# Performance work log

Measured on AMD Instinct MI355X. Metric: run time of the kernel, lower is better.

The kernel has to match this reference:

```python
import jax, jax.numpy as jnp
import numpy as np

B, N, D, H = 8, 384, 256, 1024

def setup_inputs() -> dict:
    key = jax.random.key(0)
    ks = jax.random.split(key, 8)
    x = jax.random.normal(ks[0], (B, N, D), jnp.float32)
    adj = jnp.ones((B, N, N), jnp.float32)
    box_num = jax.random.randint(ks[1], (B, 1), 1, N + 1).astype(jnp.int64)
    box_num = box_num.at[0, 0].set(N)  # original code assumes max(box_num) == N
    fc1_w = jax.random.normal(ks[2], (H, D), jnp.float32) * (1.0 / np.sqrt(D))
    fc1_b = jnp.zeros((H,), jnp.float32)
    fc2_w = jax.random.normal(ks[3], (D, H), jnp.float32) * (1.0 / np.sqrt(H))
    fc2_b = jnp.zeros((D,), jnp.float32)
    learn_w = jax.random.uniform(ks[4], (D,), jnp.float32)  # uniform_(0,1) init
    return {"x": x, "adj": adj, "box_num": box_num,
            "fc1_w": fc1_w, "fc1_b": fc1_b, "fc2_w": fc2_w, "fc2_b": fc2_b,
            "learn_w": learn_w}

def reference(x, adj, box_num, fc1_w, fc1_b, fc2_w, fc2_b, learn_w):
    # mlp: fc2(relu(fc1(x)))  -> x_hat (B,N,D)
    x_hat = jnp.maximum(x @ fc1_w.T + fc1_b, 0.0) @ fc2_w.T + fc2_b
    # dynamic mask: -1 where either node i or j is padding, 0 otherwise
    valid = jnp.arange(N)[None, :] < box_num            # (B,N)
    pair_valid = valid[:, None, :] & valid[:, :, None]  # (B,N,N)
    mask = jnp.where(pair_valid, 0.0, -1.0)             # (B,N,N)
    # pairwise weighted L1 distance: einsum('bijd,d->bij', |x_i - x_j| + mask, w)
    # mask broadcasts over d, so its contribution is mask * sum(w) (same math,
    # avoids a second (B,N,N,D) materialization)
    absdiff = jnp.abs(x_hat[:, :, None, :] - x_hat[:, None, :, :])  # (B,N,N,D)
    dist = jnp.einsum('bijd,d->bij', absdiff, learn_w) + mask * jnp.sum(learn_w)
    out = jax.nn.leaky_relu(dist, negative_slope=0.01)
    out = out - jnp.max(out, axis=-1, keepdims=True)
    soft_adj = adj * jnp.exp(out)
    soft_adj = soft_adj / jnp.sum(soft_adj, axis=-1, keepdims=True) + 1e-10
    return soft_adj, x_hat
```

## Files before the change

kernel.cpp:

```cpp
#include <hip/hip_runtime.h>
#include <math.h>

#define B_ 8
#define N_ 384
#define D_ 256
#define H_ 1024

typedef __bf16 bh;
typedef __bf16 bf16x8 __attribute__((ext_vector_type(8)));
typedef float  f32x4  __attribute__((ext_vector_type(4)));
typedef _Float16 h2 __attribute__((ext_vector_type(2)));

#define LDK 40

#if __has_builtin(__builtin_amdgcn_fdot2)
#define FDOT2(a,b,c) __builtin_amdgcn_fdot2((a),(b),(c),false)
#else
#define FDOT2(a,b,c) ((c) + (float)(a).x*(float)(b).x + (float)(a).y*(float)(b).y)
#endif

__device__ inline h2 habs2(h2 x) {
    unsigned u = __builtin_bit_cast(unsigned, x) & 0x7fff7fffu;
    return __builtin_bit_cast(h2, u);
}

__device__ inline void split2(float v, bh& h, bh& l) {
    h = (bh)v;
    l = (bh)(v - (float)h);
}

__device__ inline int load_boxnum(const int* __restrict__ p, int b) {
    bool is64 = ((p[1] | p[3] | p[5] | p[7]) == 0);
    return is64 ? p[2 * b] : p[b];
}

__global__ __launch_bounds__(256) void gemm1_kernel(
        const float* __restrict__ A,
        const float* __restrict__ W,
        const float* __restrict__ bias,
        bh* __restrict__ Ch, bh* __restrict__ Cl)
{
    __shared__ __align__(16) bh AhS[64 * LDK], AlS[64 * LDK], WhS[64 * LDK], WlS[64 * LDK];
    const int tid = threadIdx.x;
    const int m0 = blockIdx.y * 64, n0 = blockIdx.x * 64;
    const int r = tid >> 2, kq = (tid & 3) * 8;
    const int lane = tid & 63, wv_ = tid >> 6;
    const int wm = (wv_ & 1) * 32, wn = (wv_ >> 1) * 32;
    const int l15 = lane & 15, q = lane >> 4;

    f32x4 acc[2][2] = {};
    for (int k0 = 0; k0 < 256; k0 += 32) {
        const float* ap = A + (size_t)(m0 + r) * 256 + k0 + kq;
        const float* wp = W + (size_t)(n0 + r) * 256 + k0 + kq;
        float4 a0 = *(const float4*)ap;
        float4 a1 = *(const float4*)(ap + 4);
        float4 w0 = *(const float4*)wp;
        float4 w1 = *(const float4*)(wp + 4);
        float av[8] = {a0.x, a0.y, a0.z, a0.w, a1.x, a1.y, a1.z, a1.w};
        float wf[8] = {w0.x, w0.y, w0.z, w0.w, w1.x, w1.y, w1.z, w1.w};
        bf16x8 ah, al, wh, wl;
        #pragma unroll
        for (int i = 0; i < 8; i++) {
            bh h, l;
            split2(av[i], h, l); ah[i] = h; al[i] = l;
            split2(wf[i], h, l); wh[i] = h; wl[i] = l;
        }
        __syncthreads();
        *(bf16x8*)&AhS[r * LDK + kq] = ah;  *(bf16x8*)&AlS[r * LDK + kq] = al;
        *(bf16x8*)&WhS[r * LDK + kq] = wh;  *(bf16x8*)&WlS[r * LDK + kq] = wl;
        __syncthreads();
        bf16x8 fah[2], fal[2], fwh[2], fwl[2];
        #pragma unroll
        for (int mi = 0; mi < 2; mi++) {
            int row = wm + mi * 16 + l15;
            fah[mi] = *(const bf16x8*)&AhS[row * LDK + q * 8];
            fal[mi] = *(const bf16x8*)&AlS[row * LDK + q * 8];
        }
        #pragma unroll
        for (int ni = 0; ni < 2; ni++) {
            int row = wn + ni * 16 + l15;
            fwh[ni] = *(const bf16x8*)&WhS[row * LDK + q * 8];
            fwl[ni] = *(const bf16x8*)&WlS[row * LDK + q * 8];
        }
        #pragma unroll
        for (int mi = 0; mi < 2; mi++)
            #pragma unroll
            for (int ni = 0; ni < 2; ni++) {
                acc[mi][ni] = __builtin_amdgcn_mfma_f32_16x16x32_bf16(fah[mi], fwh[ni], acc[mi][ni], 0, 0, 0);
                acc[mi][ni] = __builtin_amdgcn_mfma_f32_16x16x32_bf16(fah[mi], fwl[ni], acc[mi][ni], 0, 0, 0);
                acc[mi][ni] = __builtin_amdgcn_mfma_f32_16x16x32_bf16(fal[mi], fwh[ni], acc[mi][ni], 0, 0, 0);
            }
    }
    #pragma unroll
    for (int ni = 0; ni < 2; ni++) {
        int col = n0 + wn + ni * 16 + l15;
        float bb = bias[col];
        #pragma unroll
        for (int mi = 0; mi < 2; mi++)
            #pragma unroll
            for (int reg = 0; reg < 4; reg++) {
                int row = m0 + wm + mi * 16 + q * 4 + reg;
                float v = fmaxf(acc[mi][ni][reg] + bb, 0.f);
                bh h, l; split2(v, h, l);
                size_t off = (size_t)row * H_ + col;
                Ch[off] = h; Cl[off] = l;
            }
    }
}

__global__ __launch_bounds__(128) void gemm2_kernel(
        const bh* __restrict__ Ah_, const bh* __restrict__ Al_,
        const float* __restrict__ W,
        const float* __restrict__ bias,
        float* __restrict__ C)
{
    __shared__ __align__(16) bh AhS[64 * LDK], AlS[64 * LDK], WhS[32 * LDK], WlS[32 * LDK];
    const int tid = threadIdx.x;
    const int m0 = blockIdx.y * 64, n0 = blockIdx.x * 32;
    const int lane = tid & 63, wv_ = tid >> 6;
    const int wm = wv_ * 32;
    const int l15 = lane & 15, q = lane >> 4;
    const int ra = tid >> 1, ka = (tid & 1) * 16;
    const int rw = tid >> 2, kw = (tid & 3) * 8;

    f32x4 acc[2][2] = {};
    for (int k0 = 0; k0 < 1024; k0 += 32) {
        const bh* ahp = Ah_ + (size_t)(m0 + ra) * H_ + k0 + ka;
        const bh* alp = Al_ + (size_t)(m0 + ra) * H_ + k0 + ka;
        bf16x8 h0 = *(const bf16x8*)ahp, h1 = *(const bf16x8*)(ahp + 8);
        bf16x8 l0 = *(const bf16x8*)alp, l1 = *(const bf16x8*)(alp + 8);
        const float* wp = W + (size_t)(n0 + rw) * H_ + k0 + kw;
        float4 w0 = *(const float4*)wp, w1 = *(const float4*)(wp + 4);
        float wf[8] = {w0.x, w0.y, w0.z, w0.w, w1.x, w1.y, w1.z, w1.w};
        bf16x8 wh, wl;
        #pragma unroll
        for (int i = 0; i < 8; i++) { bh h, l; split2(wf[i], h, l); wh[i] = h; wl[i] = l; }
        __syncthreads();
        *(bf16x8*)&AhS[ra * LDK + ka] = h0;  *(bf16x8*)&AhS[ra * LDK + ka + 8] = h1;
        *(bf16x8*)&AlS[ra * LDK + ka] = l0;  *(bf16x8*)&AlS[ra * LDK + ka + 8] = l1;
        *(bf16x8*)&WhS[rw * LDK + kw] = wh;  *(bf16x8*)&WlS[rw * LDK + kw] = wl;
        __syncthreads();
        bf16x8 fah[2], fal[2], fwh[2], fwl[2];
        #pragma unroll
        for (int mi = 0; mi < 2; mi++) {
            int row = wm + mi * 16 + l15;
            fah[mi] = *(const bf16x8*)&AhS[row * LDK + q * 8];
            fal[mi] = *(const bf16x8*)&AlS[row * LDK + q * 8];
        }
        #pragma unroll
        for (int ni = 0; ni < 2; ni++) {
            int row = ni * 16 + l15;
            fwh[ni] = *(const bf16x8*)&WhS[row * LDK + q * 8];
            fwl[ni] = *(const bf16x8*)&WlS[row * LDK + q * 8];
        }
        #pragma unroll
        for (int mi = 0; mi < 2; mi++)
            #pragma unroll
            for (int ni = 0; ni < 2; ni++) {
                acc[mi][ni] = __builtin_amdgcn_mfma_f32_16x16x32_bf16(fah[mi], fwh[ni], acc[mi][ni], 0, 0, 0);
                acc[mi][ni] = __builtin_amdgcn_mfma_f32_16x16x32_bf16(fah[mi], fwl[ni], acc[mi][ni], 0, 0, 0);
                acc[mi][ni] = __builtin_amdgcn_mfma_f32_16x16x32_bf16(fal[mi], fwh[ni], acc[mi][ni], 0, 0, 0);
            }
    }
    #pragma unroll
    for (int ni = 0; ni < 2; ni++) {
        int col = n0 + ni * 16 + l15;
        float bb = bias[col];
        #pragma unroll
        for (int mi = 0; mi < 2; mi++)
            #pragma unroll
            for (int reg = 0; reg < 4; reg++) {
                int row = m0 + wm + mi * 16 + q * 4 + reg;
                C[(size_t)row * D_ + col] = acc[mi][ni][reg] + bb;
            }
    }
}

#define DLP 68
__global__ __launch_bounds__(256) void dist_kernel(const float* __restrict__ xhat,
                                                   const float* __restrict__ w,
                                                   const int* __restrict__ box_num,
                                                   float* __restrict__ dist) {
    __shared__ __align__(16) unsigned XiU[16 * DLP];
    __shared__ __align__(16) unsigned XjU[16 * DLP];
    const int bidx = blockIdx.x;
    const int b = bidx / 21;
    int p = bidx % 21;
    int ti = 0;
    while (p >= 6 - ti) { p -= 6 - ti; ti++; }
    const int tj = ti + p;
    const int i0 = ti * 64, j0 = tj * 64;

    const int tid = threadIdx.x;
    const int tx = tid & 15, ty = tid >> 4;
    const int lane = tid & 63;
    const int r = tid >> 2, kq = (tid & 3) * 8;
    const int kq2 = (tid & 3) * 4;

    float sumw = w[lane] + w[lane + 64] + w[lane + 128] + w[lane + 192];
    #pragma unroll
    for (int off = 32; off > 0; off >>= 1) sumw += __shfl_xor(sumw, off);

    const float* xb = xhat + (size_t)b * N_ * D_;
    float acc[4][4] = {};

    for (int k0 = 0; k0 < D_; k0 += 32) {
        h2 wk2[16];
        #pragma unroll
        for (int c = 0; c < 16; c++) {
            float2 wp = *(const float2*)&w[k0 + 2 * c];
            wk2[c] = (h2){(_Float16)wp.x, (_Float16)wp.y};
        }
        const float* ip = xb + (size_t)(i0 + r) * D_ + k0 + kq;
        const float* jp = xb + (size_t)(j0 + r) * D_ + k0 + kq;
        float4 i0v = *(const float4*)ip, i1v = *(const float4*)(ip + 4);
        float4 j0v = *(const float4*)jp, j1v = *(const float4*)(jp + 4);
        float fi[8] = {i0v.x, i0v.y, i0v.z, i0v.w, i1v.x, i1v.y, i1v.z, i1v.w};
        float fj[8] = {j0v.x, j0v.y, j0v.z, j0v.w, j1v.x, j1v.y, j1v.z, j1v.w};
        __syncthreads();
        #pragma unroll
        for (int c = 0; c < 4; c++) {
            h2 hi = (h2){(_Float16)fi[2 * c], (_Float16)fi[2 * c + 1]};
            h2 hj = (h2){(_Float16)fj[2 * c], (_Float16)fj[2 * c + 1]};
            XiU[(kq2 + c) * DLP + r] = __builtin_bit_cast(unsigned, hi);
            XjU[(kq2 + c) * DLP + r] = __builtin_bit_cast(unsigned, hj);
        }
        __syncthreads();
        #pragma unroll
        for (int k2 = 0; k2 < 16; k2++) {
            uint4 ar = *(const uint4*)&XiU[k2 * DLP + ty * 4];
            uint4 br = *(const uint4*)&XjU[k2 * DLP + tx * 4];
            h2 ai[4] = {__builtin_bit_cast(h2, ar.x), __builtin_bit_cast(h2, ar.y),
                        __builtin_bit_cast(h2, ar.z), __builtin_bit_cast(h2, ar.w)};
            h2 bj[4] = {__builtin_bit_cast(h2, br.x), __builtin_bit_cast(h2, br.y),
                        __builtin_bit_cast(h2, br.z), __builtin_bit_cast(h2, br.w)};
            h2 wv = wk2[k2];
            #pragma unroll
            for (int ii = 0; ii < 4; ii++)
                #pragma unroll
                for (int jj = 0; jj < 4; jj++) {
                    h2 d = habs2(ai[ii] - bj[jj]);
                    acc[ii][jj] = FDOT2(d, wv, acc[ii][jj]);
                }
        }
    }

    const int bn = load_boxnum(box_num, b);
    float m[4][4];
    #pragma unroll
    for (int ii = 0; ii < 4; ii++) {
        int i = i0 + ty * 4 + ii;
        bool vi = i < bn;
        #pragma unroll
        for (int jj = 0; jj < 4; jj++) {
            int j = j0 + tx * 4 + jj;
            float v = acc[ii][jj];
            if (!(vi && (j < bn))) v -= sumw;
            m[ii][jj] = v > 0.f ? v : 0.01f * v;
        }
    }
    #pragma unroll
    for (int ii = 0; ii < 4; ii++) {
        int i = i0 + ty * 4 + ii;
        float4 o = {m[ii][0], m[ii][1], m[ii][2], m[ii][3]};
        *(float4*)&dist[((size_t)b * N_ + i) * N_ + j0 + tx * 4] = o;
    }
    #pragma unroll
    for (int jj = 0; jj < 4; jj++) {
        int j = j0 + tx * 4 + jj;
        float4 o = {m[0][jj], m[1][jj], m[2][jj], m[3][jj]};
        *(float4*)&dist[((size_t)b * N_ + j) * N_ + i0 + ty * 4] = o;
    }
}

__global__ __launch_bounds__(256) void softmax_kernel(float* __restrict__ sa,
                                                      const float* __restrict__ adj) {
    const int row = blockIdx.x * 4 + (threadIdx.x >> 6);
    const int t = threadIdx.x & 63;
    float* prow = sa + (size_t)row * N_;
    const float* arow = adj + (size_t)row * N_;
    float v[6];
    float m = -1e30f;
    #pragma unroll
    for (int qq = 0; qq < 6; qq++) { v[qq] = prow[t + qq * 64]; m = fmaxf(m, v[qq]); }
    #pragma unroll
    for (int off = 32; off > 0; off >>= 1) m = fmaxf(m, __shfl_xor(m, off));
    float e[6];
    float s = 0.f;
    #pragma unroll
    for (int qq = 0; qq < 6; qq++) { e[qq] = arow[t + qq * 64] * expf(v[qq] - m); s += e[qq]; }
    #pragma unroll
    for (int off = 32; off > 0; off >>= 1) s += __shfl_xor(s, off);
    float inv = 1.0f / s;
    #pragma unroll
    for (int qq = 0; qq < 6; qq++) prow[t + qq * 64] = e[qq] * inv + 1e-10f;
}

extern "C" void kernel_launch(void* const* d_in, const int* in_sizes, int n_in,
                              void* d_out, int out_size, void* d_ws, size_t ws_size,
                              hipStream_t stream) {
    const float* x       = (const float*)d_in[0];
    const float* adj     = (const float*)d_in[1];
    const int*   box_num = (const int*)d_in[2];
    const float* fc1_w   = (const float*)d_in[3];
    const float* fc1_b   = (const float*)d_in[4];
    const float* fc2_w   = (const float*)d_in[5];
    const float* fc2_b   = (const float*)d_in[6];
    const float* learn_w = (const float*)d_in[7];

    float* soft_adj = (float*)d_out;
    float* xhat     = (float*)d_out + (size_t)B_ * N_ * N_;

    const int BN = B_ * N_;
    const size_t bytes_per_row = (size_t)H_ * 2 * 2;
    long long mr = (long long)(ws_size / bytes_per_row) & ~63LL;
    int max_rows = (int)((mr > BN) ? BN : mr);
    if (max_rows < 64) max_rows = 64;
    bh* c1h = (bh*)d_ws;
    bh* c1l = c1h + (size_t)max_rows * H_;

    for (int m0 = 0; m0 < BN; m0 += max_rows) {
        int rows = BN - m0; if (rows > max_rows) rows = max_rows;
        dim3 g1(H_ / 64, rows / 64);
        gemm1_kernel<<<g1, 256, 0, stream>>>(x + (size_t)m0 * D_, fc1_w, fc1_b, c1h, c1l);
        dim3 g2(D_ / 32, rows / 64);
        gemm2_kernel<<<g2, 128, 0, stream>>>(c1h, c1l, fc2_w, fc2_b, xhat + (size_t)m0 * D_);
    }

    dist_kernel<<<B_ * 21, 256, 0, stream>>>(xhat, learn_w, box_num, soft_adj);

    softmax_kernel<<<BN / 4, 256, 0, stream>>>(soft_adj, adj);
}
```

Measured before the change: 140.5 us.

## Pre-split operands to bf16 hi/lo, widen GEMM K-tiles, restructure dist kernel

A new split kernel converts x and both weight matrices into bf16 hi/lo pairs once, so the GEMMs no longer redo the split inside their K loops. Both GEMMs now stage 64-wide K tiles per sync, and gemm2 runs 256 threads with one 16-row M tile per wave. gemm2 also writes an fp16 copy of x_hat, which the distance kernel loads in one pass into a 128-row transposed shared tile and processes with 512 threads. The cost is an extra kernel launch and more workspace, and correctness relies on ws_size being large enough for the fixed buffers.

```diff
diff --git a/kernel.cpp b/kernel.cpp
--- a/kernel.cpp
+++ b/kernel.cpp
@@ -8,10 +8,11 @@
 
 typedef __bf16 bh;
 typedef __bf16 bf16x8 __attribute__((ext_vector_type(8)));
+typedef __bf16 bf16x4 __attribute__((ext_vector_type(4)));
 typedef float  f32x4  __attribute__((ext_vector_type(4)));
 typedef _Float16 h2 __attribute__((ext_vector_type(2)));
 
-#define LDK 40
+#define LDB 72
 
 #if __has_builtin(__builtin_amdgcn_fdot2)
 #define FDOT2(a,b,c) __builtin_amdgcn_fdot2((a),(b),(c),false)
@@ -34,62 +35,83 @@
     return is64 ? p[2 * b] : p[b];
 }
 
+__global__ __launch_bounds__(256) void split3_kernel(
+        const float* __restrict__ s0, bh* __restrict__ h0, bh* __restrict__ l0, int n0,
+        const float* __restrict__ s1, bh* __restrict__ h1, bh* __restrict__ l1, int n1,
+        const float* __restrict__ s2, bh* __restrict__ h2_, bh* __restrict__ l2, int n2)
+{
+    const int total = n0 + n1 + n2;
+    for (int qd = blockIdx.x * blockDim.x + threadIdx.x; qd < total; qd += gridDim.x * blockDim.x) {
+        const float* s; bh* ph; bh* pl; int i;
+        if (qd < n0)           { s = s0; ph = h0;  pl = l0; i = qd; }
+        else if (qd < n0 + n1) { s = s1; ph = h1;  pl = l1; i = qd - n0; }
+        else                   { s = s2; ph = h2_; pl = l2; i = qd - n0 - n1; }
+        float4 v = *(const float4*)(s + 4 * (size_t)i);
+        bf16x4 hv, lv; bh hh, ll;
+        split2(v.x, hh, ll); hv[0] = hh; lv[0] = ll;
+        split2(v.y, hh, ll); hv[1] = hh; lv[1] = ll;
+        split2(v.z, hh, ll); hv[2] = hh; lv[2] = ll;
+        split2(v.w, hh, ll); hv[3] = hh; lv[3] = ll;
+        *(bf16x4*)(ph + 4 * (size_t)i) = hv;
+        *(bf16x4*)(pl + 4 * (size_t)i) = lv;
+    }
+}
+
 __global__ __launch_bounds__(256) void gemm1_kernel(
-        const float* __restrict__ A,
-        const float* __restrict__ W,
+        const bh* __restrict__ Ah_, const bh* __restrict__ Al_,
+        const bh* __restrict__ Wh_, const bh* __restrict__ Wl_,
         const float* __restrict__ bias,
         bh* __restrict__ Ch, bh* __restrict__ Cl)
 {
-    __shared__ __align__(16) bh AhS[64 * LDK], AlS[64 * LDK], WhS[64 * LDK], WlS[64 * LDK];
+    __shared__ __align__(16) bh AhS[64 * LDB], AlS[64 * LDB], WhS[64 * LDB], WlS[64 * LDB];
     const int tid = threadIdx.x;
     const int m0 = blockIdx.y * 64, n0 = blockIdx.x * 64;
-    const int r = tid >> 2, kq = (tid & 3) * 8;
+    const int r = tid >> 2, kq = (tid & 3) * 16;
     const int lane = tid & 63, wv_ = tid >> 6;
     const int wm = (wv_ & 1) * 32, wn = (wv_ >> 1) * 32;
     const int l15 = lane & 15, q = lane >> 4;
 
     f32x4 acc[2][2] = {};
-    for (int k0 = 0; k0 < 256; k0 += 32) {
-        const float* ap = A + (size_t)(m0 + r) * 256 + k0 + kq;
-        const float* wp = W + (size_t)(n0 + r) * 256 + k0 + kq;
-        float4 a0 = *(const float4*)ap;
-        float4 a1 = *(const float4*)(ap + 4);
-        float4 w0 = *(const float4*)wp;
-        float4 w1 = *(const float4*)(wp + 4);
-        float av[8] = {a0.x, a0.y, a0.z, a0.w, a1.x, a1.y, a1.z, a1.w};
-        float wf[8] = {w0.x, w0.y, w0.z, w0.w, w1.x, w1.y, w1.z, w1.w};
-        bf16x8 ah, al, wh, wl;
-        #pragma unroll
-        for (int i = 0; i < 8; i++) {
-            bh h, l;
-            split2(av[i], h, l); ah[i] = h; al[i] = l;
-            split2(wf[i], h, l); wh[i] = h; wl[i] = l;
+    for (int k0 = 0; k0 < D_; k0 += 64) {
+        const bh* pah = Ah_ + (size_t)(m0 + r) * D_ + k0 + kq;
+        const bh* pal = Al_ + (size_t)(m0 + r) * D_ + k0 + kq;
+        const bh* pwh = Wh_ + (size_t)(n0 + r) * D_ + k0 + kq;
+        const bh* pwl = Wl_ + (size_t)(n0 + r) * D_ + k0 + kq;
+        bf16x8 ah0 = *(const bf16x8*)pah, ah1 = *(const bf16x8*)(pah + 8);
+        bf16x8 al0 = *(const bf16x8*)pal, al1 = *(const bf16x8*)(pal + 8);
+        bf16x8 wh0 = *(const bf16x8*)pwh, wh1 = *(const bf16x8*)(pwh + 8);
+        bf16x8 wl0 = *(const bf16x8*)pwl, wl1 = *(const bf16x8*)(pwl + 8);
+        __syncthreads();
+        *(bf16x8*)&AhS[r * LDB + kq] = ah0;  *(bf16x8*)&AhS[r * LDB + kq + 8] = ah1;
+        *(bf16x8*)&AlS[r * LDB + kq] = al0;  *(bf16x8*)&AlS[r * LDB + kq + 8] = al1;
+        *(bf16x8*)&WhS[r * LDB + kq] = wh0;  *(bf16x8*)&WhS[r * LDB + kq + 8] = wh1;
+        *(bf16x8*)&WlS[r * LDB + kq] = wl0;  *(bf16x8*)&WlS[r * LDB + kq + 8] = wl1;
+        __syncthreads();
+        #pragma unroll
+        for (int ks = 0; ks < 2; ks++) {
+            const int kb = ks * 32 + q * 8;
+            bf16x8 fah[2], fal[2], fwh[2], fwl[2];
+            #pragma unroll
+            for (int mi = 0; mi < 2; mi++) {
+                int row = wm + mi * 16 + l15;
+                fah[mi] = *(const bf16x8*)&AhS[row * LDB + kb];
+                fal[mi] = *(const bf16x8*)&AlS[row * LDB + kb];
+            }
+            #pragma unroll
+            for (int ni = 0; ni < 2; ni++) {
+                int row = wn + ni * 16 + l15;
+                fwh[ni] = *(const bf16x8*)&WhS[row * LDB + kb];
+                fwl[ni] = *(const bf16x8*)&WlS[row * LDB + kb];
+            }
+            #pragma unroll
+            for (int mi = 0; mi < 2; mi++)
+                #pragma unroll
+                for (int ni = 0; ni < 2; ni++) {
+                    acc[mi][ni] = __builtin_amdgcn_mfma_f32_16x16x32_bf16(fah[mi], fwh[ni], acc[mi][ni], 0, 0, 0);
+                    acc[mi][ni] = __builtin_amdgcn_mfma_f32_16x16x32_bf16(fah[mi], fwl[ni], acc[mi][ni], 0, 0, 0);
+                    acc[mi][ni] = __builtin_amdgcn_mfma_f32_16x16x32_bf16(fal[mi], fwh[ni], acc[mi][ni], 0, 0, 0);
+                }
         }
-        __syncthreads();
-        *(bf16x8*)&AhS[r * LDK + kq] = ah;  *(bf16x8*)&AlS[r * LDK + kq] = al;
-        *(bf16x8*)&WhS[r * LDK + kq] = wh;  *(bf16x8*)&WlS[r * LDK + kq] = wl;
-        __syncthreads();
-        bf16x8 fah[2], fal[2], fwh[2], fwl[2];
-        #pragma unroll
-        for (int mi = 0; mi < 2; mi++) {
-            int row = wm + mi * 16 + l15;
-            fah[mi] = *(const bf16x8*)&AhS[row * LDK + q * 8];
-            fal[mi] = *(const bf16x8*)&AlS[row * LDK + q * 8];
-        }
-        #pragma unroll
-        for (int ni = 0; ni < 2; ni++) {
-            int row = wn + ni * 16 + l15;
-            fwh[ni] = *(const bf16x8*)&WhS[row * LDK + q * 8];
-            fwl[ni] = *(const bf16x8*)&WlS[row * LDK + q * 8];
-        }
-        #pragma unroll
-        for (int mi = 0; mi < 2; mi++)
-            #pragma unroll
-            for (int ni = 0; ni < 2; ni++) {
-                acc[mi][ni] = __builtin_amdgcn_mfma_f32_16x16x32_bf16(fah[mi], fwh[ni], acc[mi][ni], 0, 0, 0);
-                acc[mi][ni] = __builtin_amdgcn_mfma_f32_16x16x32_bf16(fah[mi], fwl[ni], acc[mi][ni], 0, 0, 0);
-                acc[mi][ni] = __builtin_amdgcn_mfma_f32_16x16x32_bf16(fal[mi], fwh[ni], acc[mi][ni], 0, 0, 0);
-            }
     }
     #pragma unroll
     for (int ni = 0; ni < 2; ni++) {
@@ -108,81 +130,75 @@
     }
 }
 
-__global__ __launch_bounds__(128) void gemm2_kernel(
+__global__ __launch_bounds__(256) void gemm2_kernel(
         const bh* __restrict__ Ah_, const bh* __restrict__ Al_,
-        const float* __restrict__ W,
+        const bh* __restrict__ Wh_, const bh* __restrict__ Wl_,
         const float* __restrict__ bias,
-        float* __restrict__ C)
+        float* __restrict__ C, _Float16* __restrict__ C16)
 {
-    __shared__ __align__(16) bh AhS[64 * LDK], AlS[64 * LDK], WhS[32 * LDK], WlS[32 * LDK];
+    __shared__ __align__(16) bh AhS[64 * LDB], AlS[64 * LDB], WhS[32 * LDB], WlS[32 * LDB];
     const int tid = threadIdx.x;
     const int m0 = blockIdx.y * 64, n0 = blockIdx.x * 32;
     const int lane = tid & 63, wv_ = tid >> 6;
-    const int wm = wv_ * 32;
+    const int wm = wv_ * 16;
     const int l15 = lane & 15, q = lane >> 4;
-    const int ra = tid >> 1, ka = (tid & 1) * 16;
-    const int rw = tid >> 2, kw = (tid & 3) * 8;
-
-    f32x4 acc[2][2] = {};
-    for (int k0 = 0; k0 < 1024; k0 += 32) {
-        const bh* ahp = Ah_ + (size_t)(m0 + ra) * H_ + k0 + ka;
-        const bh* alp = Al_ + (size_t)(m0 + ra) * H_ + k0 + ka;
-        bf16x8 h0 = *(const bf16x8*)ahp, h1 = *(const bf16x8*)(ahp + 8);
-        bf16x8 l0 = *(const bf16x8*)alp, l1 = *(const bf16x8*)(alp + 8);
-        const float* wp = W + (size_t)(n0 + rw) * H_ + k0 + kw;
-        float4 w0 = *(const float4*)wp, w1 = *(const float4*)(wp + 4);
-        float wf[8] = {w0.x, w0.y, w0.z, w0.w, w1.x, w1.y, w1.z, w1.w};
-        bf16x8 wh, wl;
-        #pragma unroll
-        for (int i = 0; i < 8; i++) { bh h, l; split2(wf[i], h, l); wh[i] = h; wl[i] = l; }
+    const int r = tid >> 2, kq = (tid & 3) * 16;
+    const int rw = tid >> 3, kw = (tid & 7) * 8;
+
+    f32x4 acc[2] = {};
+    for (int k0 = 0; k0 < H_; k0 += 64) {
+        const bh* pah = Ah_ + (size_t)(m0 + r) * H_ + k0 + kq;
+        const bh* pal = Al_ + (size_t)(m0 + r) * H_ + k0 + kq;
+        const bh* pwh = Wh_ + (size_t)(n0 + rw) * H_ + k0 + kw;
+        const bh* pwl = Wl_ + (size_t)(n0 + rw) * H_ + k0 + kw;
+        bf16x8 ah0 = *(const bf16x8*)pah, ah1 = *(const bf16x8*)(pah + 8);
+        bf16x8 al0 = *(const bf16x8*)pal, al1 = *(const bf16x8*)(pal + 8);
+        bf16x8 wh0 = *(const bf16x8*)pwh;
+        bf16x8 wl0 = *(const bf16x8*)pwl;
         __syncthreads();
-        *(bf16x8*)&AhS[ra * LDK + ka] = h0;  *(bf16x8*)&AhS[ra * LDK + ka + 8] = h1;
-        *(bf16x8*)&AlS[ra * LDK + ka] = l0;  *(bf16x8*)&AlS[ra * LDK + ka + 8] = l1;
-        *(bf16x8*)&WhS[rw * LDK + kw] = wh;  *(bf16x8*)&WlS[rw * LDK + kw] = wl;
+        *(bf16x8*)&AhS[r * LDB + kq] = ah0;  *(bf16x8*)&AhS[r * LDB + kq + 8] = ah1;
+        *(bf16x8*)&AlS[r * LDB + kq] = al0;  *(bf16x8*)&AlS[r * LDB + kq + 8] = al1;
+        *(bf16x8*)&WhS[rw * LDB + kw] = wh0;
+        *(bf16x8*)&WlS[rw * LDB + kw] = wl0;
         __syncthreads();
-        bf16x8 fah[2], fal[2], fwh[2], fwl[2];
-        #pragma unroll
-        for (int mi = 0; mi < 2; mi++) {
-            int row = wm + mi * 16 + l15;
-            fah[mi] = *(const bf16x8*)&AhS[row * LDK + q * 8];
-            fal[mi] = *(const bf16x8*)&AlS[row * LDK + q * 8];
+        #pragma unroll
+        for (int ks = 0; ks < 2; ks++) {
+            const int kb = ks * 32 + q * 8;
+            const int arow = wm + l15;
+            bf16x8 fah = *(const bf16x8*)&AhS[arow * LDB + kb];
+            bf16x8 fal = *(const bf16x8*)&AlS[arow * LDB + kb];
+            #pragma unroll
+            for (int ni = 0; ni < 2; ni++) {
+                int row = ni * 16 + l15;
+                bf16x8 fwh = *(const bf16x8*)&WhS[row * LDB + kb];
+                bf16x8 fwl = *(const bf16x8*)&WlS[row * LDB + kb];
+                acc[ni] = __builtin_amdgcn_mfma_f32_16x16x32_bf16(fah, fwh, acc[ni], 0, 0, 0);
+                acc[ni] = __builtin_amdgcn_mfma_f32_16x16x32_bf16(fah, fwl, acc[ni], 0, 0, 0);
+                acc[ni] = __builtin_amdgcn_mfma_f32_16x16x32_bf16(fal, fwh, acc[ni], 0, 0, 0);
+            }
         }
-        #pragma unroll
-        for (int ni = 0; ni < 2; ni++) {
-            int row = ni * 16 + l15;
-            fwh[ni] = *(const bf16x8*)&WhS[row * LDK + q * 8];
-            fwl[ni] = *(const bf16x8*)&WlS[row * LDK + q * 8];
-        }
-        #pragma unroll
-        for (int mi = 0; mi < 2; mi++)
-            #pragma unroll
-            for (int ni = 0; ni < 2; ni++) {
-                acc[mi][ni] = __builtin_amdgcn_mfma_f32_16x16x32_bf16(fah[mi], fwh[ni], acc[mi][ni], 0, 0, 0);
-                acc[mi][ni] = __builtin_amdgcn_mfma_f32_16x16x32_bf16(fah[mi], fwl[ni], acc[mi][ni], 0, 0, 0);
-                acc[mi][ni] = __builtin_amdgcn_mfma_f32_16x16x32_bf16(fal[mi], fwh[ni], acc[mi][ni], 0, 0, 0);
-            }
     }
     #pragma unroll
     for (int ni = 0; ni < 2; ni++) {
         int col = n0 + ni * 16 + l15;
         float bb = bias[col];
         #pragma unroll
-        for (int mi = 0; mi < 2; mi++)
-            #pragma unroll
-            for (int reg = 0; reg < 4; reg++) {
-                int row = m0 + wm + mi * 16 + q * 4 + reg;
-                C[(size_t)row * D_ + col] = acc[mi][ni][reg] + bb;
-            }
-    }
-}
-
-#define DLP 68
-__global__ __launch_bounds__(256) void dist_kernel(const float* __restrict__ xhat,
+        for (int reg = 0; reg < 4; reg++) {
+            int row = m0 + wm + q * 4 + reg;
+            float v = acc[ni][reg] + bb;
+            C[(size_t)row * D_ + col] = v;
+            C16[(size_t)row * D_ + col] = (_Float16)v;
+        }
+    }
+}
+
+#define DLX 132
+__global__ __launch_bounds__(512) void dist_kernel(const _Float16* __restrict__ xh16,
                                                    const float* __restrict__ w,
                                                    const int* __restrict__ box_num,
                                                    float* __restrict__ dist) {
-    __shared__ __align__(16) unsigned XiU[16 * DLP];
-    __shared__ __align__(16) unsigned XjU[16 * DLP];
+    __shared__ __align__(16) unsigned X[128 * DLX];
+    __shared__ unsigned WkS[128];
     const int bidx = blockIdx.x;
     const int b = bidx / 21;
     int p = bidx % 21;
@@ -190,70 +206,61 @@
     while (p >= 6 - ti) { p -= 6 - ti; ti++; }
     const int tj = ti + p;
     const int i0 = ti * 64, j0 = tj * 64;
-
     const int tid = threadIdx.x;
-    const int tx = tid & 15, ty = tid >> 4;
     const int lane = tid & 63;
-    const int r = tid >> 2, kq = (tid & 3) * 8;
-    const int kq2 = (tid & 3) * 4;
 
     float sumw = w[lane] + w[lane + 64] + w[lane + 128] + w[lane + 192];
     #pragma unroll
     for (int off = 32; off > 0; off >>= 1) sumw += __shfl_xor(sumw, off);
 
-    const float* xb = xhat + (size_t)b * N_ * D_;
-    float acc[4][4] = {};
-
-    for (int k0 = 0; k0 < D_; k0 += 32) {
-        h2 wk2[16];
-        #pragma unroll
-        for (int c = 0; c < 16; c++) {
-            float2 wp = *(const float2*)&w[k0 + 2 * c];
-            wk2[c] = (h2){(_Float16)wp.x, (_Float16)wp.y};
-        }
-        const float* ip = xb + (size_t)(i0 + r) * D_ + k0 + kq;
-        const float* jp = xb + (size_t)(j0 + r) * D_ + k0 + kq;
-        float4 i0v = *(const float4*)ip, i1v = *(const float4*)(ip + 4);
-        float4 j0v = *(const float4*)jp, j1v = *(const float4*)(jp + 4);
-        float fi[8] = {i0v.x, i0v.y, i0v.z, i0v.w, i1v.x, i1v.y, i1v.z, i1v.w};
-        float fj[8] = {j0v.x, j0v.y, j0v.z, j0v.w, j1v.x, j1v.y, j1v.z, j1v.w};
-        __syncthreads();
-        #pragma unroll
-        for (int c = 0; c < 4; c++) {
-            h2 hi = (h2){(_Float16)fi[2 * c], (_Float16)fi[2 * c + 1]};
-            h2 hj = (h2){(_Float16)fj[2 * c], (_Float16)fj[2 * c + 1]};
-            XiU[(kq2 + c) * DLP + r] = __builtin_bit_cast(unsigned, hi);
-            XjU[(kq2 + c) * DLP + r] = __builtin_bit_cast(unsigned, hj);
-        }
-        __syncthreads();
-        #pragma unroll
-        for (int k2 = 0; k2 < 16; k2++) {
-            uint4 ar = *(const uint4*)&XiU[k2 * DLP + ty * 4];
-            uint4 br = *(const uint4*)&XjU[k2 * DLP + tx * 4];
-            h2 ai[4] = {__builtin_bit_cast(h2, ar.x), __builtin_bit_cast(h2, ar.y),
-                        __builtin_bit_cast(h2, ar.z), __builtin_bit_cast(h2, ar.w)};
-            h2 bj[4] = {__builtin_bit_cast(h2, br.x), __builtin_bit_cast(h2, br.y),
-                        __builtin_bit_cast(h2, br.z), __builtin_bit_cast(h2, br.w)};
-            h2 wv = wk2[k2];
-            #pragma unroll
-            for (int ii = 0; ii < 4; ii++)
-                #pragma unroll
-                for (int jj = 0; jj < 4; jj++) {
-                    h2 d = habs2(ai[ii] - bj[jj]);
-                    acc[ii][jj] = FDOT2(d, wv, acc[ii][jj]);
-                }
-        }
+    if (tid < 128) {
+        float2 wp = *(const float2*)&w[2 * tid];
+        h2 wv = {(_Float16)wp.x, (_Float16)wp.y};
+        WkS[tid] = __builtin_bit_cast(unsigned, wv);
+    }
+
+    const int sr = tid >> 2, koff = (tid & 3) * 64;
+    const int grow = (sr < 64) ? (i0 + sr) : (j0 + sr - 64);
+    const _Float16* src = xh16 + ((size_t)b * N_ + grow) * D_ + koff;
+    #pragma unroll
+    for (int ld = 0; ld < 8; ld++) {
+        uint4 v = *(const uint4*)(src + ld * 8);
+        int k2 = (koff >> 1) + ld * 4;
+        X[(k2 + 0) * DLX + sr] = v.x;
+        X[(k2 + 1) * DLX + sr] = v.y;
+        X[(k2 + 2) * DLX + sr] = v.z;
+        X[(k2 + 3) * DLX + sr] = v.w;
+    }
+    __syncthreads();
+
+    const int tx = tid & 31, ty = tid >> 5;
+    float acc[4][2] = {};
+    #pragma unroll 4
+    for (int k2 = 0; k2 < 128; k2++) {
+        uint4 av = *(const uint4*)&X[k2 * DLX + ty * 4];
+        uint2 bv = *(const uint2*)&X[k2 * DLX + 64 + tx * 2];
+        h2 wv = __builtin_bit_cast(h2, WkS[k2]);
+        h2 ai[4] = {__builtin_bit_cast(h2, av.x), __builtin_bit_cast(h2, av.y),
+                    __builtin_bit_cast(h2, av.z), __builtin_bit_cast(h2, av.w)};
+        h2 bj[2] = {__builtin_bit_cast(h2, bv.x), __builtin_bit_cast(h2, bv.y)};
+        #pragma unroll
+        for (int ii = 0; ii < 4; ii++)
+            #pragma unroll
+            for (int jj = 0; jj < 2; jj++) {
+                h2 d = habs2(ai[ii] - bj[jj]);
+                acc[ii][jj] = FDOT2(d, wv, acc[ii][jj]);
+            }
     }
 
     const int bn = load_boxnum(box_num, b);
-    float m[4][4];
+    float m[4][2];
     #pragma unroll
     for (int ii = 0; ii < 4; ii++) {
         int i = i0 + ty * 4 + ii;
         bool vi = i < bn;
         #pragma unroll
-        for (int jj = 0; jj < 4; jj++) {
-            int j = j0 + tx * 4 + jj;
+        for (int jj = 0; jj < 2; jj++) {
+            int j = j0 + tx * 2 + jj;
             float v = acc[ii][jj];
             if (!(vi && (j < bn))) v -= sumw;
             m[ii][jj] = v > 0.f ? v : 0.01f * v;
@@ -262,12 +269,12 @@
     #pragma unroll
     for (int ii = 0; ii < 4; ii++) {
         int i = i0 + ty * 4 + ii;
-        float4 o = {m[ii][0], m[ii][1], m[ii][2], m[ii][3]};
-        *(float4*)&dist[((size_t)b * N_ + i) * N_ + j0 + tx * 4] = o;
-    }
-    #pragma unroll
-    for (int jj = 0; jj < 4; jj++) {
-        int j = j0 + tx * 4 + jj;
+        float2 o = {m[ii][0], m[ii][1]};
+        *(float2*)&dist[((size_t)b * N_ + i) * N_ + j0 + tx * 2] = o;
+    }
+    #pragma unroll
+    for (int jj = 0; jj < 2; jj++) {
+        int j = j0 + tx * 2 + jj;
         float4 o = {m[0][jj], m[1][jj], m[2][jj], m[3][jj]};
         *(float4*)&dist[((size_t)b * N_ + j) * N_ + i0 + ty * 4] = o;
     }
@@ -312,22 +319,48 @@
     float* xhat     = (float*)d_out + (size_t)B_ * N_ * N_;
 
     const int BN = B_ * N_;
-    const size_t bytes_per_row = (size_t)H_ * 2 * 2;
-    long long mr = (long long)(ws_size / bytes_per_row) & ~63LL;
-    int max_rows = (int)((mr > BN) ? BN : mr);
-    if (max_rows < 64) max_rows = 64;
-    bh* c1h = (bh*)d_ws;
-    bh* c1l = c1h + (size_t)max_rows * H_;
-
+
+    bh* w1h = (bh*)d_ws;
+    bh* w1l = w1h + (size_t)H_ * D_;
+    bh* w2h = w1l + (size_t)H_ * D_;
+    bh* w2l = w2h + (size_t)D_ * H_;
+    _Float16* xh16 = (_Float16*)(w2l + (size_t)D_ * H_);
+    bh* cbase = (bh*)(xh16 + (size_t)BN * D_);
+    const size_t fixed_bytes = (size_t)4 * H_ * D_ * 2 + (size_t)BN * D_ * 2;
+    const size_t per_row = (size_t)(D_ * 2 + H_ * 2) * 2;
+
+    long long avail = (long long)ws_size - (long long)fixed_bytes;
+    long long mr = (avail > 0) ? (avail / (long long)per_row) : 0;
+    if (mr > BN) mr = BN;
+    mr &= ~63LL;
+    if (mr < 64) mr = 64;
+    const int max_rows = (int)mr;
+
+    bool first = true;
     for (int m0 = 0; m0 < BN; m0 += max_rows) {
         int rows = BN - m0; if (rows > max_rows) rows = max_rows;
+        bh* xh  = cbase;
+        bh* xl  = xh + (size_t)max_rows * D_;
+        bh* c1h = xl + (size_t)max_rows * D_;
+        bh* c1l = c1h + (size_t)max_rows * H_;
+
+        int n0q = rows * D_ / 4;
+        int n1q = first ? (H_ * D_ / 4) : 0;
+        int n2q = first ? (D_ * H_ / 4) : 0;
+        split3_kernel<<<512, 256, 0, stream>>>(
+            x + (size_t)m0 * D_, xh, xl, n0q,
+            fc1_w, w1h, w1l, n1q,
+            fc2_w, w2h, w2l, n2q);
+
         dim3 g1(H_ / 64, rows / 64);
-        gemm1_kernel<<<g1, 256, 0, stream>>>(x + (size_t)m0 * D_, fc1_w, fc1_b, c1h, c1l);
+        gemm1_kernel<<<g1, 256, 0, stream>>>(xh, xl, w1h, w1l, fc1_b, c1h, c1l);
         dim3 g2(D_ / 32, rows / 64);
-        gemm2_kernel<<<g2, 128, 0, stream>>>(c1h, c1l, fc2_w, fc2_b, xhat + (size_t)m0 * D_);
-    }
-
-    dist_kernel<<<B_ * 21, 256, 0, stream>>>(xhat, learn_w, box_num, soft_adj);
+        gemm2_kernel<<<g2, 256, 0, stream>>>(c1h, c1l, w2h, w2l, fc2_b,
+                                             xhat + (size_t)m0 * D_, xh16 + (size_t)m0 * D_);
+        first = false;
+    }
+
+    dist_kernel<<<B_ * 21, 512, 0, stream>>>(xh16, learn_w, box_num, soft_adj);
 
     softmax_kernel<<<BN / 4, 256, 0, stream>>>(soft_adj, adj);
 }
```

Measured after the change: 123.9 us. 11.9% less time.
